# Performance work log

Hardware: AMD Instinct MI355X
Metric: run time of the kernel (lower is better)

Reference implementation:

```python
import jax, jax.numpy as jnp
import numpy as np

B, T, F, H = 32, 2048, 256, 256  # batch, steps, features, n_hidden
FORGET_BIAS = 1.0  # BasicLSTMCell default


def setup_inputs() -> dict:
    key = jax.random.key(0)
    k1, k2, k3, k4, k5 = jax.random.split(key, 5)
    u = lambda k, shape: jax.random.uniform(k, shape, jnp.float32, -0.1, 0.1)
    return {
        "x": jax.random.normal(k1, (B, T, F), jnp.float32),
        "W_fw": u(k2, (F + H, 4 * H)),  # BasicLSTMCell single kernel [in+hidden, 4H]
        "b_fw": jnp.zeros((4 * H,), jnp.float32),
        "W_bw": u(k3, (F + H, 4 * H)),
        "b_bw": jnp.zeros((4 * H,), jnp.float32),
    }


def _lstm_dir(x, W, b):
    # x: [B,T,F]; W: [F+H,4H]; gate order i, j, f, o (BasicLSTMCell)
    Wx, Wh = W[:F], W[F:]
    xg = jnp.einsum('btf,fg->btg', x, Wx) + b  # precompute input contribution [B,T,4H]

    def step(carry, g_t):
        c, h = carry
        gates = g_t + h @ Wh
        i, j, f, o = jnp.split(gates, 4, axis=-1)
        c = c * jax.nn.sigmoid(f + FORGET_BIAS) + jax.nn.sigmoid(i) * jnp.tanh(j)
        h = jnp.tanh(c) * jax.nn.sigmoid(o)
        return (c, h), h

    init = (jnp.zeros((x.shape[0], H), x.dtype), jnp.zeros((x.shape[0], H), x.dtype))
    _, hs = jax.lax.scan(step, init, jnp.swapaxes(xg, 0, 1))  # [T,B,H]
    return jnp.swapaxes(hs, 0, 1)  # [B,T,H]


def reference(x, W_fw, b_fw, W_bw, b_bw):
    out_fw = _lstm_dir(x, W_fw, b_fw)
    out_bw = _lstm_dir(x[:, ::-1], W_bw, b_bw)[:, ::-1]  # backward direction
    return jnp.concatenate([out_fw, out_bw], axis=-1)  # [B,T,2H]
```

## Files before the change

kernel.cpp:

```cpp
#include <hip/hip_runtime.h>

#define T_LEN 2048

typedef _Float16 f16x8 __attribute__((ext_vector_type(8)));
typedef float f32x4 __attribute__((ext_vector_type(4)));
typedef unsigned int u32;

__device__ __forceinline__ float sigm(float v) { return 1.f / (1.f + __expf(-v)); }

__device__ __forceinline__ void* swzA(_Float16* base, int row, int k) {
  int byte = row * 1024 + k * 2;
  byte ^= (row & 7) << 4;
  return (void*)((char*)base + byte);
}

__device__ __forceinline__ void issue3_sc0(const u32* p1, const u32* p2,
                                           const u32* p3, u32& a, u32& b,
                                           u32& c) {
  asm volatile(
      "global_load_dword %0, %3, off sc0\n\t"
      "global_load_dword %1, %4, off sc0\n\t"
      "global_load_dword %2, %5, off sc0"
      : "=&v"(a), "=&v"(b), "=&v"(c)
      : "v"(p1), "v"(p2), "v"(p3)
      : "memory");
}
__device__ __forceinline__ void wait3(u32& a, u32& b, u32& c) {
  asm volatile("s_waitcnt vmcnt(0)" : "+v"(a), "+v"(b), "+v"(c)::"memory");
}

__global__ __launch_bounds__(1024, 4) void bilstm_kernel(
    const float* __restrict__ x, const float* __restrict__ Wfw,
    const float* __restrict__ bfw, const float* __restrict__ Wbw,
    const float* __restrict__ bbw, float* __restrict__ out,
    u32* __restrict__ hglob) {
  const int bid = blockIdx.x;
  if ((bid & 7) >= 4) return;
  const int g = bid & 7;
  const int m = bid >> 3;
  const int dir = g >> 1, bh = g & 1;
  const int tid = threadIdx.x;
  const int w = tid >> 6;
  const int lane = tid & 63;
  const int l15 = lane & 15, l4 = lane >> 4;

  const float* W = dir ? Wbw : Wfw;
  const float* bias = dir ? bbw : bfw;

  __shared__ _Float16 Alds[16 * 512];
  __shared__ float Glds[16 * 260];

  const int p = w >> 2;
  const int cbase = p * 64 + (w & 3) * 16;
  const int gcol = p * 256 + 64 * m + (w & 3) * 16 + l15;
  f16x8 wB[16];
#pragma unroll
  for (int kk = 0; kk < 16; ++kk) {
    const int kb = kk * 32 + l4 * 8;
    f16x8 h;
#pragma unroll
    for (int j = 0; j < 8; ++j) h[j] = (_Float16)W[(kb + j) * 1024 + gcol];
    wB[kk] = h;
  }
  const float bcol = bias[gcol] + ((p == 2) ? 1.f : 0.f);

  const int cs = tid >> 6;
  const int cd = tid & 63;
  float c = 0.f;
  bool use_mall = false;

  u32* Hg = hglob + g * (2 * 16 * 256);
  const int pd1 = 64 * ((m + 1) & 3) + cd;
  const int pd2 = 64 * ((m + 2) & 3) + cd;
  const int pd3 = 64 * ((m + 3) & 3) + cd;
  u32* my0 = Hg + (0 * 16 + cs) * 256 + 64 * m + cd;
  u32* my1 = Hg + (1 * 16 + cs) * 256 + 64 * m + cd;

  {
    uint2 z = {0u, 0u};
    *(uint2*)swzA(Alds, cs, 256 + 4 * cd) = z;
  }
  const int tx0 = dir ? (T_LEN - 1) : 0;
  f32x4 xv = *(const f32x4*)(x + (((bh * 16 + cs) * T_LEN + tx0) << 8) + 4 * cd);

  for (int t = 0; t < T_LEN; ++t) {
    const int tx = dir ? (T_LEN - 1 - t) : t;

    {
      union { _Float16 h[4]; uint2 q; } ux;
#pragma unroll
      for (int j = 0; j < 4; ++j) ux.h[j] = (_Float16)xv[j];
      *(uint2*)swzA(Alds, cs, 4 * cd) = ux.q;
    }
    __syncthreads();

    const u32 want = (u32)t;
    u32* Hp = Hg + (((t & 1) ^ 1) * 16 + cs) * 256;
    u32 s1 = 0, s2 = 0, s3 = 0;
    if (t > 0) issue3_sc0(Hp + pd1, Hp + pd2, Hp + pd3, s1, s2, s3);

    {
      const int tn = (t + 1 < T_LEN) ? t + 1 : t;
      const int txn = dir ? (T_LEN - 1 - tn) : tn;
      xv = *(const f32x4*)(x + (((bh * 16 + cs) * T_LEN + txn) << 8) + 4 * cd);
    }

    f32x4 acc = {bcol, bcol, bcol, bcol};
#pragma unroll
    for (int kk = 0; kk < 8; ++kk) {
      f16x8 a = *(const f16x8*)swzA(Alds, l15, kk * 32 + l4 * 8);
      acc = __builtin_amdgcn_mfma_f32_16x16x32_f16(a, wB[kk], acc, 0, 0, 0);
    }
#pragma unroll
    for (int q = 0; q < 4; ++q) {
      if (q == m) {
        f16x8 a0 = *(const f16x8*)swzA(Alds, l15, (8 + 2 * q) * 32 + l4 * 8);
        acc = __builtin_amdgcn_mfma_f32_16x16x32_f16(a0, wB[8 + 2 * q], acc, 0, 0, 0);
        f16x8 a1 = *(const f16x8*)swzA(Alds, l15, (9 + 2 * q) * 32 + l4 * 8);
        acc = __builtin_amdgcn_mfma_f32_16x16x32_f16(a1, wB[9 + 2 * q], acc, 0, 0, 0);
      }
    }

    if (t > 0) {
      wait3(s1, s2, s3);
      int tries = 0;
      while ((s1 >> 16) != want || (s2 >> 16) != want || (s3 >> 16) != want) {
        if (use_mall) {
          s1 = __hip_atomic_load(Hp + pd1, __ATOMIC_RELAXED, __HIP_MEMORY_SCOPE_AGENT);
          s2 = __hip_atomic_load(Hp + pd2, __ATOMIC_RELAXED, __HIP_MEMORY_SCOPE_AGENT);
          s3 = __hip_atomic_load(Hp + pd3, __ATOMIC_RELAXED, __HIP_MEMORY_SCOPE_AGENT);
        } else {
          issue3_sc0(Hp + pd1, Hp + pd2, Hp + pd3, s1, s2, s3);
          wait3(s1, s2, s3);
          if (++tries > 24) use_mall = true;
        }
      }
      *(unsigned short*)swzA(Alds, cs, 256 + pd1) = (unsigned short)(s1 & 0xffffu);
      *(unsigned short*)swzA(Alds, cs, 256 + pd2) = (unsigned short)(s2 & 0xffffu);
      *(unsigned short*)swzA(Alds, cs, 256 + pd3) = (unsigned short)(s3 & 0xffffu);
    }
    __syncthreads();

#pragma unroll
    for (int q = 0; q < 4; ++q) {
      if (q != m) {
        f16x8 a0 = *(const f16x8*)swzA(Alds, l15, (8 + 2 * q) * 32 + l4 * 8);
        acc = __builtin_amdgcn_mfma_f32_16x16x32_f16(a0, wB[8 + 2 * q], acc, 0, 0, 0);
        f16x8 a1 = *(const f16x8*)swzA(Alds, l15, (9 + 2 * q) * 32 + l4 * 8);
        acc = __builtin_amdgcn_mfma_f32_16x16x32_f16(a1, wB[9 + 2 * q], acc, 0, 0, 0);
      }
    }

    {
      float* gw = Glds + cbase + l15;
      const int r = l4 * 4;
#pragma unroll
      for (int v = 0; v < 4; ++v) gw[(r + v) * 260] = acc[v];
    }
    __syncthreads();

    const float* Gp = Glds + cs * 260 + cd;
    const float gi = Gp[0 * 64], gj = Gp[1 * 64], gf = Gp[2 * 64], go = Gp[3 * 64];
    c = c * sigm(gf) + sigm(gi) * (2.f * sigm(gj + gj) - 1.f);
    const float h = (2.f * sigm(c + c) - 1.f) * sigm(go);

    union { _Float16 hf; unsigned short us; } cv;
    cv.hf = (_Float16)h;
    u32* pub = (t & 1) ? my1 : my0;
    __hip_atomic_store(pub, (((u32)(t + 1)) << 16) | (u32)cv.us,
                       __ATOMIC_RELAXED, __HIP_MEMORY_SCOPE_AGENT);
    *(unsigned short*)swzA(Alds, cs, 256 + 64 * m + cd) = cv.us;
    __builtin_nontemporal_store(
        h, out + (((bh * 16 + cs) * T_LEN + tx) << 9) + dir * 256 + 64 * m + cd);
  }
}

extern "C" void kernel_launch(void* const* d_in, const int* in_sizes, int n_in,
                              void* d_out, int out_size, void* d_ws,
                              size_t ws_size, hipStream_t stream) {
  const float* x = (const float*)d_in[0];
  const float* Wfw = (const float*)d_in[1];
  const float* bfw = (const float*)d_in[2];
  const float* Wbw = (const float*)d_in[3];
  const float* bbw = (const float*)d_in[4];
  float* out = (float*)d_out;

  u32* hglob = (u32*)d_ws;
  (void)hipMemsetAsync(hglob, 0, 4 * 2 * 16 * 256 * sizeof(u32), stream);

  bilstm_kernel<<<dim3(32), dim3(1024), 0, stream>>>(x, Wfw, bfw, Wbw, bbw, out,
                                                     hglob);
}
```

Measured before the change: 4.916 ms.

## Double-buffer LDS, compute gates in registers via shuffles, split mailbox local/global

```diff
diff --git a/kernel.cpp b/kernel.cpp
--- a/kernel.cpp
+++ b/kernel.cpp
@@ -14,6 +14,9 @@
   return (void*)((char*)base + byte);
 }
 
+__device__ __forceinline__ void lstore(u32* p, u32 v) {
+  asm volatile("global_store_dword %0, %1, off" ::"v"(p), "v"(v) : "memory");
+}
 __device__ __forceinline__ void issue3_sc0(const u32* p1, const u32* p2,
                                            const u32* p3, u32& a, u32& b,
                                            u32& c) {
@@ -25,7 +28,7 @@
       : "v"(p1), "v"(p2), "v"(p3)
       : "memory");
 }
-__device__ __forceinline__ void wait3(u32& a, u32& b, u32& c) {
+__device__ __forceinline__ void wait_vm0(u32& a, u32& b, u32& c) {
   asm volatile("s_waitcnt vmcnt(0)" : "+v"(a), "+v"(b), "+v"(c)::"memory");
 }
 
@@ -33,7 +36,7 @@
     const float* __restrict__ x, const float* __restrict__ Wfw,
     const float* __restrict__ bfw, const float* __restrict__ Wbw,
     const float* __restrict__ bbw, float* __restrict__ out,
-    u32* __restrict__ hglob) {
+    u32* __restrict__ gmbox, u32* __restrict__ lmbox, u32* __restrict__ flags) {
   const int bid = blockIdx.x;
   if ((bid & 7) >= 4) return;
   const int g = bid & 7;
@@ -43,61 +46,93 @@
   const int w = tid >> 6;
   const int lane = tid & 63;
   const int l15 = lane & 15, l4 = lane >> 4;
+  const int p = l15 >> 2;
 
   const float* W = dir ? Wbw : Wfw;
   const float* bias = dir ? bbw : bfw;
 
-  __shared__ _Float16 Alds[16 * 512];
-  __shared__ float Glds[16 * 260];
-
-  const int p = w >> 2;
-  const int cbase = p * 64 + (w & 3) * 16;
-  const int gcol = p * 256 + 64 * m + (w & 3) * 16 + l15;
+  __shared__ _Float16 A[2][16 * 512];
+
+  const int qblk = (p == 1) ? 2 : ((p == 2) ? 1 : p);
+  const int gcol = qblk * 256 + 64 * m + 4 * w + (l15 & 3);
   f16x8 wB[16];
 #pragma unroll
   for (int kk = 0; kk < 16; ++kk) {
     const int kb = kk * 32 + l4 * 8;
-    f16x8 h;
-#pragma unroll
-    for (int j = 0; j < 8; ++j) h[j] = (_Float16)W[(kb + j) * 1024 + gcol];
-    wB[kk] = h;
-  }
-  const float bcol = bias[gcol] + ((p == 2) ? 1.f : 0.f);
-
-  const int cs = tid >> 6;
-  const int cd = tid & 63;
-  float c = 0.f;
-  bool use_mall = false;
-
-  u32* Hg = hglob + g * (2 * 16 * 256);
+    f16x8 hld;
+#pragma unroll
+    for (int j = 0; j < 8; ++j) hld[j] = (_Float16)W[(kb + j) * 1024 + gcol];
+    wB[kk] = hld;
+  }
+  const float bcol = bias[gcol] + ((p == 1) ? 1.f : 0.f);
+
+  u32* Gm = gmbox + g * (2 * 16 * 256);
+  u32* Lm = lmbox + g * (2 * 16 * 256);
+
+  const int cs = w, cd = lane;
   const int pd1 = 64 * ((m + 1) & 3) + cd;
   const int pd2 = 64 * ((m + 2) & 3) + cd;
   const int pd3 = 64 * ((m + 3) & 3) + cd;
-  u32* my0 = Hg + (0 * 16 + cs) * 256 + 64 * m + cd;
-  u32* my1 = Hg + (1 * 16 + cs) * 256 + 64 * m + cd;
-
+
+#pragma unroll
+  for (int b = 0; b < 2; ++b) {
+    u32* Lb = Lm + (b * 16 + cs) * 256;
+    lstore(Lb + pd1, 0u);
+    lstore(Lb + pd2, 0u);
+    lstore(Lb + pd3, 0u);
+  }
   {
     uint2 z = {0u, 0u};
-    *(uint2*)swzA(Alds, cs, 256 + 4 * cd) = z;
-  }
+    *(uint2*)swzA(A[0], cs, 256 + 4 * cd) = z;
+  }
+  __syncthreads();
+  if (tid == 0) {
+    __hip_atomic_store(flags + g * 4 + m, 1, __ATOMIC_RELEASE,
+                       __HIP_MEMORY_SCOPE_AGENT);
+    int got;
+    do {
+      got = 0;
+      for (int q = 0; q < 4; ++q)
+        got += __hip_atomic_load(flags + g * 4 + q, __ATOMIC_ACQUIRE,
+                                 __HIP_MEMORY_SCOPE_AGENT);
+    } while (got < 4);
+  }
+  __syncthreads();
+
   const int tx0 = dir ? (T_LEN - 1) : 0;
   f32x4 xv = *(const f32x4*)(x + (((bh * 16 + cs) * T_LEN + tx0) << 8) + 4 * cd);
 
+  float c[4] = {0.f, 0.f, 0.f, 0.f};
+  unsigned short hb[4] = {0, 0, 0, 0};
+  bool use_global = false;
+  const bool s1b = (l15 & 4) != 0;
+  const bool s2b = (l15 & 8) != 0;
+
   for (int t = 0; t < T_LEN; ++t) {
+    const int bufc = t & 1;
     const int tx = dir ? (T_LEN - 1 - t) : t;
+    _Float16* Ab = A[bufc];
 
     {
-      union { _Float16 h[4]; uint2 q; } ux;
-#pragma unroll
-      for (int j = 0; j < 4; ++j) ux.h[j] = (_Float16)xv[j];
-      *(uint2*)swzA(Alds, cs, 4 * cd) = ux.q;
-    }
-    __syncthreads();
-
+      union { _Float16 h4[4]; uint2 q; } ux;
+#pragma unroll
+      for (int j = 0; j < 4; ++j) ux.h4[j] = (_Float16)xv[j];
+      *(uint2*)swzA(Ab, cs, 4 * cd) = ux.q;
+    }
+
+    u32 s1 = 0, s2 = 0, s3 = 0;
     const u32 want = (u32)t;
-    u32* Hp = Hg + (((t & 1) ^ 1) * 16 + cs) * 256;
-    u32 s1 = 0, s2 = 0, s3 = 0;
-    if (t > 0) issue3_sc0(Hp + pd1, Hp + pd2, Hp + pd3, s1, s2, s3);
+    u32* Lp = Lm + ((bufc ^ 1) * 16 + cs) * 256;
+    u32* Gp = Gm + ((bufc ^ 1) * 16 + cs) * 256;
+    if (t > 0) {
+      if (p == 0) {
+        const int kd = 256 + 64 * m + 4 * w + l15;
+#pragma unroll
+        for (int v = 0; v < 4; ++v)
+          *(unsigned short*)swzA(Ab, 4 * l4 + v, kd) = hb[v];
+      }
+      if (!use_global) issue3_sc0(Lp + pd1, Lp + pd2, Lp + pd3, s1, s2, s3);
+    }
 
     {
       const int tn = (t + 1 < T_LEN) ? t + 1 : t;
@@ -105,73 +140,68 @@
       xv = *(const f32x4*)(x + (((bh * 16 + cs) * T_LEN + txn) << 8) + 4 * cd);
     }
 
+    if (t > 0) {
+      if (!use_global) {
+        wait_vm0(s1, s2, s3);
+        int tries = 0;
+        while ((s1 >> 16) != want || (s2 >> 16) != want || (s3 >> 16) != want) {
+          if (++tries > 64) { use_global = true; break; }
+          issue3_sc0(Lp + pd1, Lp + pd2, Lp + pd3, s1, s2, s3);
+          wait_vm0(s1, s2, s3);
+        }
+      }
+      if (use_global) {
+        for (;;) {
+          s1 = __hip_atomic_load(Gp + pd1, __ATOMIC_RELAXED, __HIP_MEMORY_SCOPE_AGENT);
+          s2 = __hip_atomic_load(Gp + pd2, __ATOMIC_RELAXED, __HIP_MEMORY_SCOPE_AGENT);
+          s3 = __hip_atomic_load(Gp + pd3, __ATOMIC_RELAXED, __HIP_MEMORY_SCOPE_AGENT);
+          if ((s1 >> 16) == want && (s2 >> 16) == want && (s3 >> 16) == want) break;
+        }
+      }
+      *(unsigned short*)swzA(Ab, cs, 256 + pd1) = (unsigned short)(s1 & 0xffffu);
+      *(unsigned short*)swzA(Ab, cs, 256 + pd2) = (unsigned short)(s2 & 0xffffu);
+      *(unsigned short*)swzA(Ab, cs, 256 + pd3) = (unsigned short)(s3 & 0xffffu);
+    }
+    __syncthreads();
+
     f32x4 acc = {bcol, bcol, bcol, bcol};
 #pragma unroll
-    for (int kk = 0; kk < 8; ++kk) {
-      f16x8 a = *(const f16x8*)swzA(Alds, l15, kk * 32 + l4 * 8);
+    for (int kk = 0; kk < 16; ++kk) {
+      f16x8 a = *(const f16x8*)swzA(Ab, l15, kk * 32 + l4 * 8);
       acc = __builtin_amdgcn_mfma_f32_16x16x32_f16(a, wB[kk], acc, 0, 0, 0);
     }
-#pragma unroll
-    for (int q = 0; q < 4; ++q) {
-      if (q == m) {
-        f16x8 a0 = *(const f16x8*)swzA(Alds, l15, (8 + 2 * q) * 32 + l4 * 8);
-        acc = __builtin_amdgcn_mfma_f32_16x16x32_f16(a0, wB[8 + 2 * q], acc, 0, 0, 0);
-        f16x8 a1 = *(const f16x8*)swzA(Alds, l15, (9 + 2 * q) * 32 + l4 * 8);
-        acc = __builtin_amdgcn_mfma_f32_16x16x32_f16(a1, wB[9 + 2 * q], acc, 0, 0, 0);
-      }
-    }
-
-    if (t > 0) {
-      wait3(s1, s2, s3);
-      int tries = 0;
-      while ((s1 >> 16) != want || (s2 >> 16) != want || (s3 >> 16) != want) {
-        if (use_mall) {
-          s1 = __hip_atomic_load(Hp + pd1, __ATOMIC_RELAXED, __HIP_MEMORY_SCOPE_AGENT);
-          s2 = __hip_atomic_load(Hp + pd2, __ATOMIC_RELAXED, __HIP_MEMORY_SCOPE_AGENT);
-          s3 = __hip_atomic_load(Hp + pd3, __ATOMIC_RELAXED, __HIP_MEMORY_SCOPE_AGENT);
-        } else {
-          issue3_sc0(Hp + pd1, Hp + pd2, Hp + pd3, s1, s2, s3);
-          wait3(s1, s2, s3);
-          if (++tries > 24) use_mall = true;
-        }
-      }
-      *(unsigned short*)swzA(Alds, cs, 256 + pd1) = (unsigned short)(s1 & 0xffffu);
-      *(unsigned short*)swzA(Alds, cs, 256 + pd2) = (unsigned short)(s2 & 0xffffu);
-      *(unsigned short*)swzA(Alds, cs, 256 + pd3) = (unsigned short)(s3 & 0xffffu);
-    }
-    __syncthreads();
-
-#pragma unroll
-    for (int q = 0; q < 4; ++q) {
-      if (q != m) {
-        f16x8 a0 = *(const f16x8*)swzA(Alds, l15, (8 + 2 * q) * 32 + l4 * 8);
-        acc = __builtin_amdgcn_mfma_f32_16x16x32_f16(a0, wB[8 + 2 * q], acc, 0, 0, 0);
-        f16x8 a1 = *(const f16x8*)swzA(Alds, l15, (9 + 2 * q) * 32 + l4 * 8);
-        acc = __builtin_amdgcn_mfma_f32_16x16x32_f16(a1, wB[9 + 2 * q], acc, 0, 0, 0);
-      }
-    }
-
-    {
-      float* gw = Glds + cbase + l15;
-      const int r = l4 * 4;
-#pragma unroll
-      for (int v = 0; v < 4; ++v) gw[(r + v) * 260] = acc[v];
-    }
-    __syncthreads();
-
-    const float* Gp = Glds + cs * 260 + cd;
-    const float gi = Gp[0 * 64], gj = Gp[1 * 64], gf = Gp[2 * 64], go = Gp[3 * 64];
-    c = c * sigm(gf) + sigm(gi) * (2.f * sigm(gj + gj) - 1.f);
-    const float h = (2.f * sigm(c + c) - 1.f) * sigm(go);
-
-    union { _Float16 hf; unsigned short us; } cv;
-    cv.hf = (_Float16)h;
-    u32* pub = (t & 1) ? my1 : my0;
-    __hip_atomic_store(pub, (((u32)(t + 1)) << 16) | (u32)cv.us,
-                       __ATOMIC_RELAXED, __HIP_MEMORY_SCOPE_AGENT);
-    *(unsigned short*)swzA(Alds, cs, 256 + 64 * m + cd) = cv.us;
-    __builtin_nontemporal_store(
-        h, out + (((bh * 16 + cs) * T_LEN + tx) << 9) + dir * 256 + 64 * m + cd);
+
+    const u32 stamp = ((u32)(t + 1)) << 16;
+    const int dim64 = 64 * m + 4 * w + l15;
+    u32* Lq = Lm + (bufc * 16) * 256;
+    u32* Gq = Gm + (bufc * 16) * 256;
+#pragma unroll
+    for (int v = 0; v < 4; ++v) {
+      float A0 = acc[v];
+      float A1 = __shfl_xor(A0, 4);
+      float A2 = __shfl_xor(A0, 8);
+      float A3 = __shfl_xor(A1, 8);
+      float B0 = s1b ? A1 : A0, B1 = s1b ? A0 : A1;
+      float B2 = s1b ? A3 : A2, B3 = s1b ? A2 : A3;
+      float gi = s2b ? B2 : B0;
+      float gf = s2b ? B3 : B1;
+      float gj = s2b ? B0 : B2;
+      float go = s2b ? B1 : B3;
+      c[v] = c[v] * sigm(gf) + sigm(gi) * (2.f * sigm(gj + gj) - 1.f);
+      float h = (2.f * sigm(c[v] + c[v]) - 1.f) * sigm(go);
+      if (p == 0) {
+        union { _Float16 hf; unsigned short us; } cv;
+        cv.hf = (_Float16)h;
+        hb[v] = cv.us;
+        const int seq = 4 * l4 + v;
+        const int li = seq * 256 + dim64;
+        lstore(Lq + li, stamp | (u32)cv.us);
+        __hip_atomic_store(Gq + li, stamp | (u32)cv.us,
+                           __ATOMIC_RELAXED, __HIP_MEMORY_SCOPE_AGENT);
+        __builtin_nontemporal_store(
+            h, out + (((bh * 16 + seq) * T_LEN + tx) << 9) + dir * 256 + dim64);
+      }
+    }
   }
 }
 
@@ -185,9 +215,11 @@
   const float* bbw = (const float*)d_in[4];
   float* out = (float*)d_out;
 
-  u32* hglob = (u32*)d_ws;
-  (void)hipMemsetAsync(hglob, 0, 4 * 2 * 16 * 256 * sizeof(u32), stream);
+  u32* gmbox = (u32*)d_ws;
+  u32* flags = (u32*)((char*)d_ws + 128 * 1024);
+  u32* lmbox = (u32*)((char*)d_ws + 132 * 1024);
+  (void)hipMemsetAsync(d_ws, 0, 132 * 1024, stream);
 
   bilstm_kernel<<<dim3(32), dim3(1024), 0, stream>>>(x, Wfw, bfw, Wbw, bbw, out,
-                                                     hglob);
-}
+                                                     gmbox, lmbox, flags);
+}
```

After: 12.34 ms. 151% more time.

## Use MALL-coherent polling loads, shrink grid to 16 blocks, issue poll before barrier

Applied to the files above, without the earlier changes.

```diff
diff --git a/kernel.cpp b/kernel.cpp
--- a/kernel.cpp
+++ b/kernel.cpp
@@ -14,13 +14,13 @@
   return (void*)((char*)base + byte);
 }
 
-__device__ __forceinline__ void issue3_sc0(const u32* p1, const u32* p2,
-                                           const u32* p3, u32& a, u32& b,
-                                           u32& c) {
+__device__ __forceinline__ void issue3_mall(const u32* p1, const u32* p2,
+                                            const u32* p3, u32& a, u32& b,
+                                            u32& c) {
   asm volatile(
-      "global_load_dword %0, %3, off sc0\n\t"
-      "global_load_dword %1, %4, off sc0\n\t"
-      "global_load_dword %2, %5, off sc0"
+      "global_load_dword %0, %3, off sc0 sc1\n\t"
+      "global_load_dword %1, %4, off sc0 sc1\n\t"
+      "global_load_dword %2, %5, off sc0 sc1"
       : "=&v"(a), "=&v"(b), "=&v"(c)
       : "v"(p1), "v"(p2), "v"(p3)
       : "memory");
@@ -34,10 +34,8 @@
     const float* __restrict__ bfw, const float* __restrict__ Wbw,
     const float* __restrict__ bbw, float* __restrict__ out,
     u32* __restrict__ hglob) {
-  const int bid = blockIdx.x;
-  if ((bid & 7) >= 4) return;
-  const int g = bid & 7;
-  const int m = bid >> 3;
+  const int g = blockIdx.x & 3;
+  const int m = blockIdx.x >> 2;
   const int dir = g >> 1, bh = g & 1;
   const int tid = threadIdx.x;
   const int w = tid >> 6;
@@ -67,7 +65,6 @@
   const int cs = tid >> 6;
   const int cd = tid & 63;
   float c = 0.f;
-  bool use_mall = false;
 
   u32* Hg = hglob + g * (2 * 16 * 256);
   const int pd1 = 64 * ((m + 1) & 3) + cd;
@@ -87,17 +84,18 @@
     const int tx = dir ? (T_LEN - 1 - t) : t;
 
     {
-      union { _Float16 h[4]; uint2 q; } ux;
+      union { _Float16 h4[4]; uint2 q; } ux;
 #pragma unroll
-      for (int j = 0; j < 4; ++j) ux.h[j] = (_Float16)xv[j];
+      for (int j = 0; j < 4; ++j) ux.h4[j] = (_Float16)xv[j];
       *(uint2*)swzA(Alds, cs, 4 * cd) = ux.q;
     }
-    __syncthreads();
 
     const u32 want = (u32)t;
-    u32* Hp = Hg + (((t & 1) ^ 1) * 16 + cs) * 256;
+    const u32* Hp = Hg + (((t & 1) ^ 1) * 16 + cs) * 256;
     u32 s1 = 0, s2 = 0, s3 = 0;
-    if (t > 0) issue3_sc0(Hp + pd1, Hp + pd2, Hp + pd3, s1, s2, s3);
+    if (t > 0) issue3_mall(Hp + pd1, Hp + pd2, Hp + pd3, s1, s2, s3);
+
+    __syncthreads();
 
     {
       const int tn = (t + 1 < T_LEN) ? t + 1 : t;
@@ -123,17 +121,9 @@
 
     if (t > 0) {
       wait3(s1, s2, s3);
-      int tries = 0;
       while ((s1 >> 16) != want || (s2 >> 16) != want || (s3 >> 16) != want) {
-        if (use_mall) {
-          s1 = __hip_atomic_load(Hp + pd1, __ATOMIC_RELAXED, __HIP_MEMORY_SCOPE_AGENT);
-          s2 = __hip_atomic_load(Hp + pd2, __ATOMIC_RELAXED, __HIP_MEMORY_SCOPE_AGENT);
-          s3 = __hip_atomic_load(Hp + pd3, __ATOMIC_RELAXED, __HIP_MEMORY_SCOPE_AGENT);
-        } else {
-          issue3_sc0(Hp + pd1, Hp + pd2, Hp + pd3, s1, s2, s3);
-          wait3(s1, s2, s3);
-          if (++tries > 24) use_mall = true;
-        }
+        issue3_mall(Hp + pd1, Hp + pd2, Hp + pd3, s1, s2, s3);
+        wait3(s1, s2, s3);
       }
       *(unsigned short*)swzA(Alds, cs, 256 + pd1) = (unsigned short)(s1 & 0xffffu);
       *(unsigned short*)swzA(Alds, cs, 256 + pd2) = (unsigned short)(s2 & 0xffffu);
@@ -166,8 +156,7 @@
 
     union { _Float16 hf; unsigned short us; } cv;
     cv.hf = (_Float16)h;
-    u32* pub = (t & 1) ? my1 : my0;
-    __hip_atomic_store(pub, (((u32)(t + 1)) << 16) | (u32)cv.us,
+    __hip_atomic_store((t & 1) ? my1 : my0, (((u32)(t + 1)) << 16) | (u32)cv.us,
                        __ATOMIC_RELAXED, __HIP_MEMORY_SCOPE_AGENT);
     *(unsigned short*)swzA(Alds, cs, 256 + 64 * m + cd) = cv.us;
     __builtin_nontemporal_store(
@@ -188,6 +177,6 @@
   u32* hglob = (u32*)d_ws;
   (void)hipMemsetAsync(hglob, 0, 4 * 2 * 16 * 256 * sizeof(u32), stream);
 
-  bilstm_kernel<<<dim3(32), dim3(1024), 0, stream>>>(x, Wfw, bfw, Wbw, bbw, out,
+  bilstm_kernel<<<dim3(16), dim3(1024), 0, stream>>>(x, Wfw, bfw, Wbw, bbw, out,
                                                      hglob);
 }
```

Result: faster. 4.815 ms (-2.1%).
